# Performance work log

Measured on AMD Instinct MI355X. Metric: run time of the kernel, lower is better.

Reference implementation:

```python
import jax, jax.numpy as jnp
import numpy as np

BATCH, FIELD_DIM, EMBED_DIM = 16384, 2048, 64


def setup_inputs() -> dict:
    key = jax.random.key(0)
    k1, k2, k3 = jax.random.split(key, 3)
    x = jax.random.normal(k1, (BATCH, FIELD_DIM), dtype=jnp.float32)
    w = jax.random.normal(k2, (FIELD_DIM, 1), dtype=jnp.float32) * 0.02
    b = jnp.zeros((1,), dtype=jnp.float32)
    # FM factor matrix (xavier-normal-ish scale)
    v = jax.random.normal(k3, (FIELD_DIM, EMBED_DIM), dtype=jnp.float32) * (
        (2.0 / (FIELD_DIM + EMBED_DIM)) ** 0.5
    )
    return {"x": x, "w": w, "b": b, "v": v}


def reference(x, w, b, v):
    # First-order linear term: [B, 1]
    linear = x @ w + b
    # Second-order FM term, algebraic reformulation of the O(n^2) pairwise loop:
    # sum_{i<j} <v_i, v_j> x_i x_j = 0.5 * sum_k [(x @ v)_k^2 - (x^2 @ v^2)_k]
    xv = x @ v                       # [B, K]
    x2v2 = (x * x) @ (v * v)         # [B, K]
    second_order = 0.5 * jnp.sum(xv * xv - x2v2, axis=-1, keepdims=True)  # [B, 1]
    return jax.nn.sigmoid(linear + second_order)
```

## Files before the change

kernel.cpp:

```cpp
#include <hip/hip_runtime.h>
#include <stdint.h>

#define FD 2048

typedef short short8 __attribute__((ext_vector_type(8)));
typedef float f32x4 __attribute__((ext_vector_type(4)));
typedef unsigned short ushort_t;

__device__ __forceinline__ unsigned bf16_rne(float f) {
  unsigned u = __float_as_uint(f);
  return (u + 0x7FFFu + ((u >> 16) & 1u)) >> 16;
}

__global__ __launch_bounds__(256) void fm_prep(
    const float* __restrict__ v, ushort_t* __restrict__ hi,
    ushort_t* __restrict__ lo, float* __restrict__ s2t)
{
  int bid = blockIdx.x;
  if (bid < 512) {
    int t = bid * 256 + threadIdx.x;
    int j    = t & 7;
    int lane = (t >> 3) & 63;
    int c    = (t >> 9) & 3;
    int s    = t >> 11;
    int k    = s * 32 + ((lane >> 4) << 3) + j;
    int col  = (c << 4) + (lane & 15);
    float val = v[k * 64 + col];
    unsigned hb = bf16_rne(val);
    float hf = __uint_as_float(hb << 16);
    unsigned lb = bf16_rne(val - hf);
    hi[t] = (ushort_t)hb;
    lo[t] = (ushort_t)lb;
  } else {
    int k = (bid - 512) * 256 + threadIdx.x;
    const float4* row = (const float4*)(v + k * 64);
    float s = 0.f;
    #pragma unroll
    for (int i = 0; i < 16; ++i) {
      float4 q = row[i];
      s += q.x * q.x + q.y * q.y + q.z * q.z + q.w * q.w;
    }
    s2t[k] = s;
  }
}

__device__ __forceinline__ void cvt_row(
    const float4& A0, const float4& A1,
    const float4& W0, const float4& W1,
    const float4& S0, const float4& S1,
    short8& H, short8& L, float& lin, float& q)
{
  float f[8]  = {A0.x, A0.y, A0.z, A0.w, A1.x, A1.y, A1.z, A1.w};
  float fw[8] = {W0.x, W0.y, W0.z, W0.w, W1.x, W1.y, W1.z, W1.w};
  float fs[8] = {S0.x, S0.y, S0.z, S0.w, S1.x, S1.y, S1.z, S1.w};
  #pragma unroll
  for (int j = 0; j < 8; ++j) {
    unsigned h = bf16_rne(f[j]);
    H[j] = (short)h;
    L[j] = (short)bf16_rne(f[j] - __uint_as_float(h << 16));
    lin = fmaf(f[j], fw[j], lin);
    q   = fmaf(f[j] * f[j], fs[j], q);
  }
}

#define MF(accv, a, b) accv = __builtin_amdgcn_mfma_f32_16x16x32_bf16(a, b, accv, 0, 0, 0)

__global__ __launch_bounds__(512, 4) void fm_main(
    const float* __restrict__ x, const float* __restrict__ w,
    const float* __restrict__ bptr, const short8* __restrict__ vhi,
    const short8* __restrict__ vlo, const float* __restrict__ s2t,
    float* __restrict__ out)
{
  __shared__ float lds_w[FD];
  __shared__ float lds_s[FD];
  __shared__ float lds_xv[32][64];
  __shared__ float lds_lin[32];
  __shared__ float lds_q[32];

  const int tid = threadIdx.x;
  const int wv  = tid >> 6;
  const int l   = tid & 63;
  const int l15 = l & 15;
  const int lk  = l >> 4;
  const int R   = blockIdx.x << 5;
  const int kbase = wv << 8;

  {
    float* z = &lds_xv[0][0];
    #pragma unroll
    for (int i = tid; i < 32 * 64; i += 512) z[i] = 0.f;
    if (tid < 32) { lds_lin[tid] = 0.f; lds_q[tid] = 0.f; }
    *(float4*)&lds_w[tid << 2] = *(const float4*)(w + (tid << 2));
    *(float4*)&lds_s[tid << 2] = *(const float4*)(s2t + (tid << 2));
  }
  __syncthreads();

  const float* px0 = x + (size_t)(R + l15) * FD + kbase + (lk << 3);
  const float* px1 = px0 + (size_t)16 * FD;
  const int wsoff = kbase + (lk << 3);
  const short8* pb = vhi + (size_t)wv * 2048 + l;
  const short8* pl = vlo + (size_t)wv * 2048 + l;

  f32x4 acc[2][4];
  #pragma unroll
  for (int t = 0; t < 2; ++t)
    #pragma unroll
    for (int c = 0; c < 4; ++c)
      acc[t][c] = (f32x4){0.f, 0.f, 0.f, 0.f};

  float lin0 = 0.f, lin1 = 0.f, q0 = 0.f, q1 = 0.f;

  short8 cah0, cal0, cah1, cal1;
  {
    float4 a0 = *(const float4*)(px0);
    float4 a1 = *(const float4*)(px0 + 4);
    float4 b0 = *(const float4*)(px1);
    float4 b1 = *(const float4*)(px1 + 4);
    float4 wa = *(const float4*)&lds_w[wsoff];
    float4 wb = *(const float4*)&lds_w[wsoff + 4];
    float4 sa = *(const float4*)&lds_s[wsoff];
    float4 sb = *(const float4*)&lds_s[wsoff + 4];
    cvt_row(a0, a1, wa, wb, sa, sb, cah0, cal0, lin0, q0);
    cvt_row(b0, b1, wa, wb, sa, sb, cah1, cal1, lin1, q1);
  }

  #pragma unroll
  for (int st = 0; st < 8; ++st) {
    float4 na0, na1, nb0, nb1;
    if (st < 7) {
      const int nko = (st + 1) << 5;
      na0 = *(const float4*)(px0 + nko);
      na1 = *(const float4*)(px0 + nko + 4);
      nb0 = *(const float4*)(px1 + nko);
      nb1 = *(const float4*)(px1 + nko + 4);
    }

    short8 bh0 = pb[st * 256 + 0];
    short8 bh1 = pb[st * 256 + 64];
    short8 bh2 = pb[st * 256 + 128];
    short8 bh3 = pb[st * 256 + 192];

    MF(acc[0][0], cah0, bh0); MF(acc[0][1], cah0, bh1);
    MF(acc[0][2], cah0, bh2); MF(acc[0][3], cah0, bh3);
    MF(acc[1][0], cah1, bh0); MF(acc[1][1], cah1, bh1);
    MF(acc[1][2], cah1, bh2); MF(acc[1][3], cah1, bh3);
    MF(acc[0][0], cal0, bh0); MF(acc[0][1], cal0, bh1);
    MF(acc[0][2], cal0, bh2); MF(acc[0][3], cal0, bh3);
    MF(acc[1][0], cal1, bh0); MF(acc[1][1], cal1, bh1);
    MF(acc[1][2], cal1, bh2); MF(acc[1][3], cal1, bh3);

    short8 bl0 = pl[st * 256 + 0];
    short8 bl1 = pl[st * 256 + 64];
    short8 bl2 = pl[st * 256 + 128];
    short8 bl3 = pl[st * 256 + 192];

    MF(acc[0][0], cah0, bl0); MF(acc[0][1], cah0, bl1);
    MF(acc[0][2], cah0, bl2); MF(acc[0][3], cah0, bl3);
    MF(acc[1][0], cah1, bl0); MF(acc[1][1], cah1, bl1);
    MF(acc[1][2], cah1, bl2); MF(acc[1][3], cah1, bl3);

    if (st < 7) {
      const int nws = wsoff + ((st + 1) << 5);
      float4 wa = *(const float4*)&lds_w[nws];
      float4 wb = *(const float4*)&lds_w[nws + 4];
      float4 sa = *(const float4*)&lds_s[nws];
      float4 sb = *(const float4*)&lds_s[nws + 4];
      cvt_row(na0, na1, wa, wb, sa, sb, cah0, cal0, lin0, q0);
      cvt_row(nb0, nb1, wa, wb, sa, sb, cah1, cal1, lin1, q1);
    }
  }

  lin0 += __shfl_xor(lin0, 16, 64); lin0 += __shfl_xor(lin0, 32, 64);
  lin1 += __shfl_xor(lin1, 16, 64); lin1 += __shfl_xor(lin1, 32, 64);
  q0   += __shfl_xor(q0,   16, 64); q0   += __shfl_xor(q0,   32, 64);
  q1   += __shfl_xor(q1,   16, 64); q1   += __shfl_xor(q1,   32, 64);
  if (lk == 0) {
    atomicAdd(&lds_lin[l15],      lin0);
    atomicAdd(&lds_lin[16 + l15], lin1);
    atomicAdd(&lds_q[l15],        q0);
    atomicAdd(&lds_q[16 + l15],   q1);
  }

  #pragma unroll
  for (int t = 0; t < 2; ++t)
    #pragma unroll
    for (int c = 0; c < 4; ++c)
      #pragma unroll
      for (int j = 0; j < 4; ++j)
        atomicAdd(&lds_xv[t * 16 + lk * 4 + j][c * 16 + l15], acc[t][c][j]);

  __syncthreads();

  {
    const int row = tid >> 4;
    const int cg  = tid & 15;
    float4 s = *(const float4*)&lds_xv[row][cg << 2];
    float ss = s.x * s.x + s.y * s.y + s.z * s.z + s.w * s.w;
    ss += __shfl_xor(ss, 1, 64);
    ss += __shfl_xor(ss, 2, 64);
    ss += __shfl_xor(ss, 4, 64);
    ss += __shfl_xor(ss, 8, 64);
    if (cg == 0) {
      float z = lds_lin[row] + bptr[0] + 0.5f * (ss - lds_q[row]);
      out[R + row] = 1.f / (1.f + expf(-z));
    }
  }
}

extern "C" void kernel_launch(void* const* d_in, const int* in_sizes, int n_in,
                              void* d_out, int out_size, void* d_ws, size_t ws_size,
                              hipStream_t stream) {
  const float* x = (const float*)d_in[0];
  const float* w = (const float*)d_in[1];
  const float* b = (const float*)d_in[2];
  const float* v = (const float*)d_in[3];
  float* out = (float*)d_out;

  ushort_t* hi = (ushort_t*)d_ws;
  ushort_t* lo = hi + FD * 64;
  float*    s2 = (float*)((char*)d_ws + (size_t)FD * 64 * 2 * sizeof(ushort_t));

  fm_prep<<<520, 256, 0, stream>>>(v, hi, lo, s2);
  fm_main<<<512, 512, 0, stream>>>(x, w, b, (const short8*)hi, (const short8*)lo, s2, out);
}
```

Baseline: 246.0 us.

## Deepen software pipeline: prefetch x two stages ahead and V fragments one ahead

Restructures the main loop so raw x rows are loaded two K-steps ahead into a double buffer and the V hi/lo fragments one step ahead, with bf16 conversion done at the start of each step. The aim is to hide global-load latency behind MFMA work. This raises register pressure, so the launch-bounds occupancy hint drops from 4 to 3 blocks per CU, which trades occupancy for more in-flight loads per wave.

Result: no change. 244.8 us (-0.5%).

```diff
diff --git a/kernel.cpp b/kernel.cpp
--- a/kernel.cpp
+++ b/kernel.cpp
@@ -65,7 +65,7 @@
 
 #define MF(accv, a, b) accv = __builtin_amdgcn_mfma_f32_16x16x32_bf16(a, b, accv, 0, 0, 0)
 
-__global__ __launch_bounds__(512, 4) void fm_main(
+__global__ __launch_bounds__(512, 3) void fm_main(
     const float* __restrict__ x, const float* __restrict__ w,
     const float* __restrict__ bptr, const short8* __restrict__ vhi,
     const short8* __restrict__ vlo, const float* __restrict__ s2t,
@@ -110,35 +110,34 @@
 
   float lin0 = 0.f, lin1 = 0.f, q0 = 0.f, q1 = 0.f;
 
-  short8 cah0, cal0, cah1, cal1;
-  {
-    float4 a0 = *(const float4*)(px0);
-    float4 a1 = *(const float4*)(px0 + 4);
-    float4 b0 = *(const float4*)(px1);
-    float4 b1 = *(const float4*)(px1 + 4);
-    float4 wa = *(const float4*)&lds_w[wsoff];
-    float4 wb = *(const float4*)&lds_w[wsoff + 4];
-    float4 sa = *(const float4*)&lds_s[wsoff];
-    float4 sb = *(const float4*)&lds_s[wsoff + 4];
-    cvt_row(a0, a1, wa, wb, sa, sb, cah0, cal0, lin0, q0);
-    cvt_row(b0, b1, wa, wb, sa, sb, cah1, cal1, lin1, q1);
-  }
+  float4 xa[2][2], xb[2][2];
+  short8 bh0, bh1, bh2, bh3, bl0, bl1, bl2, bl3;
+
+  xa[0][0] = *(const float4*)(px0);
+  xa[0][1] = *(const float4*)(px0 + 4);
+  xb[0][0] = *(const float4*)(px1);
+  xb[0][1] = *(const float4*)(px1 + 4);
+  bh0 = pb[0];  bh1 = pb[64];  bh2 = pb[128];  bh3 = pb[192];
+  bl0 = pl[0];  bl1 = pl[64];  bl2 = pl[128];  bl3 = pl[192];
+  xa[1][0] = *(const float4*)(px0 + 32);
+  xa[1][1] = *(const float4*)(px0 + 36);
+  xb[1][0] = *(const float4*)(px1 + 32);
+  xb[1][1] = *(const float4*)(px1 + 36);
 
   #pragma unroll
   for (int st = 0; st < 8; ++st) {
-    float4 na0, na1, nb0, nb1;
-    if (st < 7) {
-      const int nko = (st + 1) << 5;
-      na0 = *(const float4*)(px0 + nko);
-      na1 = *(const float4*)(px0 + nko + 4);
-      nb0 = *(const float4*)(px1 + nko);
-      nb1 = *(const float4*)(px1 + nko + 4);
-    }
-
-    short8 bh0 = pb[st * 256 + 0];
-    short8 bh1 = pb[st * 256 + 64];
-    short8 bh2 = pb[st * 256 + 128];
-    short8 bh3 = pb[st * 256 + 192];
+    const int cur = st & 1;
+
+    short8 cah0, cal0, cah1, cal1;
+    {
+      const int ws = wsoff + (st << 5);
+      float4 wa = *(const float4*)&lds_w[ws];
+      float4 wb = *(const float4*)&lds_w[ws + 4];
+      float4 sa = *(const float4*)&lds_s[ws];
+      float4 sb = *(const float4*)&lds_s[ws + 4];
+      cvt_row(xa[cur][0], xa[cur][1], wa, wb, sa, sb, cah0, cal0, lin0, q0);
+      cvt_row(xb[cur][0], xb[cur][1], wa, wb, sa, sb, cah1, cal1, lin1, q1);
+    }
 
     MF(acc[0][0], cah0, bh0); MF(acc[0][1], cah0, bh1);
     MF(acc[0][2], cah0, bh2); MF(acc[0][3], cah0, bh3);
@@ -149,24 +148,27 @@
     MF(acc[1][0], cal1, bh0); MF(acc[1][1], cal1, bh1);
     MF(acc[1][2], cal1, bh2); MF(acc[1][3], cal1, bh3);
 
-    short8 bl0 = pl[st * 256 + 0];
-    short8 bl1 = pl[st * 256 + 64];
-    short8 bl2 = pl[st * 256 + 128];
-    short8 bl3 = pl[st * 256 + 192];
-
     MF(acc[0][0], cah0, bl0); MF(acc[0][1], cah0, bl1);
     MF(acc[0][2], cah0, bl2); MF(acc[0][3], cah0, bl3);
     MF(acc[1][0], cah1, bl0); MF(acc[1][1], cah1, bl1);
     MF(acc[1][2], cah1, bl2); MF(acc[1][3], cah1, bl3);
 
     if (st < 7) {
-      const int nws = wsoff + ((st + 1) << 5);
-      float4 wa = *(const float4*)&lds_w[nws];
-      float4 wb = *(const float4*)&lds_w[nws + 4];
-      float4 sa = *(const float4*)&lds_s[nws];
-      float4 sb = *(const float4*)&lds_s[nws + 4];
-      cvt_row(na0, na1, wa, wb, sa, sb, cah0, cal0, lin0, q0);
-      cvt_row(nb0, nb1, wa, wb, sa, sb, cah1, cal1, lin1, q1);
+      bh0 = pb[(st + 1) * 256 + 0];
+      bh1 = pb[(st + 1) * 256 + 64];
+      bh2 = pb[(st + 1) * 256 + 128];
+      bh3 = pb[(st + 1) * 256 + 192];
+      bl0 = pl[(st + 1) * 256 + 0];
+      bl1 = pl[(st + 1) * 256 + 64];
+      bl2 = pl[(st + 1) * 256 + 128];
+      bl3 = pl[(st + 1) * 256 + 192];
+    }
+    if (st < 6) {
+      const int ko = (st + 2) << 5;
+      xa[cur][0] = *(const float4*)(px0 + ko);
+      xa[cur][1] = *(const float4*)(px0 + ko + 4);
+      xb[cur][0] = *(const float4*)(px1 + ko);
+      xb[cur][1] = *(const float4*)(px1 + ko + 4);
     }
   }
 
```
